# Optimization experiments

Measured on AMD Instinct MI355X. Metric: run time of the kernel, lower is better.

## Reference

```python
import jax, jax.numpy as jnp
import numpy as np

NUM_EXPERTS = 64
HIDDEN_DIM = 4096
TOPK = 8


def setup_inputs() -> dict:
    key = jax.random.key(0)
    kx, kw = jax.random.split(key)
    x = jax.random.normal(kx, (16384, HIDDEN_DIM), dtype=jnp.float32)
    # nn.Linear weight is [num_experts, hidden_dim], init N(0, 0.01)
    W = jax.random.normal(kw, (NUM_EXPERTS, HIDDEN_DIM), dtype=jnp.float32) * 0.01
    return {"x": x, "W": W}


def reference(x, W):
    # router logits: [T, E]
    router_logits = jnp.einsum('th,eh->te', x, W)
    score = jnp.clip(router_logits, -2.0, 2.0)
    # top-k over experts (no router_bias branch)
    topk_scores, topk_indices = jax.lax.top_k(score, TOPK)  # [T, K]
    topk_probs = jax.nn.softmax(topk_scores, axis=-1)
    # dispatch index computation (counting-sort style)
    flat = topk_indices.reshape(-1)                      # [T*K]
    indices = jnp.argsort(flat, stable=True).astype(jnp.int32)
    tokens_per_expert = jnp.bincount(flat, length=NUM_EXPERTS)
    group_indices = jnp.cumsum(tokens_per_expert).astype(jnp.int32)
    tokens_per_expert_f = tokens_per_expert.astype(jnp.float32)
    # load-balance loss
    mean_tokens = tokens_per_expert_f / tokens_per_expert_f.sum()
    mean_prob = jax.nn.softmax(router_logits, axis=-1).mean(axis=0)
    lb_loss = jnp.dot(mean_tokens, mean_prob) * NUM_EXPERTS
    # z-loss
    zl = jnp.mean(jax.scipy.special.logsumexp(router_logits, axis=-1) ** 2)
    return (router_logits, topk_probs, topk_indices, group_indices,
            indices, tokens_per_expert, lb_loss, zl)
```

## Files before the change

### kernel.cpp

```cpp
#include <hip/hip_runtime.h>
#include <hip/hip_bf16.h>
#include <math.h>

#define NTOK   16384
#define NEXP   64
#define HID    4096
#define KSEL   8
#define EPS    7.5e-5f
#define NSPLIT 4
#define KSZ    (HID / NSPLIT)

typedef __attribute__((ext_vector_type(8))) short short8;
typedef __attribute__((ext_vector_type(4))) float f32x4;

#define O_LOGITS 0u
#define O_PROBS  1048576u
#define O_TIDX   1179648u
#define O_GROUP  1310720u
#define O_IDX    1310784u
#define O_TPE    1441856u
#define O_LB     1441920u
#define O_ZL     1441921u

#define W_LSQP    4096u
#define W_CBE     8192u
#define W_PREF    73728u
#define W_PSUM    262144u
#define W_FLAT    524288u
#define W_RNK     1048576u
#define W_WF      2097152u
#define W_PART    4194304u
#define PART_STRIDE 1048576ull

__device__ __forceinline__ unsigned short f2bf(float f) {
  unsigned u = __float_as_uint(f);
  return (unsigned short)((u + 0x7fffu + ((u >> 16) & 1u)) >> 16);
}

__device__ __forceinline__ void gload16(const void* g, void* l) {
  __builtin_amdgcn_global_load_lds((const __attribute__((address_space(1))) unsigned int*)g,
                                   (__attribute__((address_space(3))) unsigned int*)l, 16, 0, 0);
}

__global__ __launch_bounds__(256) void k_prep(const float* __restrict__ w,
                                              short8* __restrict__ wf) {
  const int kk   = blockIdx.x;
  const int nb   = threadIdx.x >> 6;
  const int lane = threadIdx.x & 63;
  const int n    = nb * 16 + (lane & 15);
  const int kb   = kk * 32 + (lane >> 4) * 8;
  const float4* wp = (const float4*)(w + (size_t)n * HID + kb);
  float4 f0 = wp[0], f1 = wp[1];
  float fv[8] = {f0.x, f0.y, f0.z, f0.w, f1.x, f1.y, f1.z, f1.w};
  short8 hi, lo;
#pragma unroll
  for (int j = 0; j < 8; ++j) {
    unsigned short h = f2bf(fv[j]);
    hi[j] = (short)h;
    float r = fv[j] - __uint_as_float((unsigned)h << 16);
    lo[j] = (short)f2bf(r);
  }
  size_t base = ((size_t)(kk * 4 + nb) * 2) * 64 + lane;
  wf[base] = hi;
  wf[base + 64] = lo;
}

__global__ __launch_bounds__(256, 4) void k_gemm(const float* __restrict__ x,
                                                 const short8* __restrict__ wf,
                                                 float* __restrict__ part) {
  __shared__ short8 wl[2][512];
  const int tid  = threadIdx.x;
  const int wv   = tid >> 6;
  const int lane = tid & 63;
  const int t0   = blockIdx.x * 64;
  const int k0   = blockIdx.y * KSZ;
  const int row  = t0 + wv * 16 + (lane & 15);

  const float* xp = x + (size_t)row * HID + k0 + (lane >> 4) * 8;
  const short8* wbase = wf + (size_t)(k0 >> 5) * 512;

  auto stage = [&](int c, int b) {
    const short8* src = wbase + (size_t)c * 512;
#pragma unroll
    for (int r = 0; r < 2; ++r) {
      const int o = r * 256 + wv * 64;
      gload16(src + o + lane, &wl[b][o]);
    }
  };

  f32x4 acc[4] = {{0,0,0,0},{0,0,0,0},{0,0,0,0},{0,0,0,0}};

  stage(0, 0);
  __syncthreads();
  const int nch = KSZ >> 5;
  for (int c = 0; c < nch; ++c) {
    const int b = c & 1;
    if (c + 1 < nch) stage(c + 1, b ^ 1);

    const float4* xq = (const float4*)(xp + c * 32);
    float4 f0 = xq[0], f1 = xq[1];
    unsigned xb[8] = {__float_as_uint(f0.x), __float_as_uint(f0.y),
                      __float_as_uint(f0.z), __float_as_uint(f0.w),
                      __float_as_uint(f1.x), __float_as_uint(f1.y),
                      __float_as_uint(f1.z), __float_as_uint(f1.w)};
    union { unsigned u[4]; short8 s; } ua, ul;
#pragma unroll
    for (int p = 0; p < 4; ++p) {
      unsigned b0 = xb[2 * p], b1 = xb[2 * p + 1];
      ua.u[p] = __builtin_amdgcn_perm(b1, b0, 0x07060302u);
      float r0 = __uint_as_float(b0) - __uint_as_float(b0 & 0xffff0000u);
      float r1 = __uint_as_float(b1) - __uint_as_float(b1 & 0xffff0000u);
      unsigned t0b = __float_as_uint(r0), t1b = __float_as_uint(r1);
      t0b += 0x7fffu + ((t0b >> 16) & 1u);
      t1b += 0x7fffu + ((t1b >> 16) & 1u);
      ul.u[p] = __builtin_amdgcn_perm(t1b, t0b, 0x07060302u);
    }
    short8 ah = ua.s, al = ul.s;

#pragma unroll
    for (int nb = 0; nb < 4; ++nb) {
      short8 bh = wl[b][nb * 128 + lane];
      short8 bl = wl[b][nb * 128 + 64 + lane];
      acc[nb] = __builtin_amdgcn_mfma_f32_16x16x32_bf16(ah, bh, acc[nb], 0, 0, 0);
      acc[nb] = __builtin_amdgcn_mfma_f32_16x16x32_bf16(al, bh, acc[nb], 0, 0, 0);
      acc[nb] = __builtin_amdgcn_mfma_f32_16x16x32_bf16(ah, bl, acc[nb], 0, 0, 0);
    }
    __syncthreads();
  }

  float* p = part + (size_t)blockIdx.y * PART_STRIDE;
  const int mrow = t0 + wv * 16 + (lane >> 4) * 4;
  const int col  = lane & 15;
#pragma unroll
  for (int nb = 0; nb < 4; ++nb)
#pragma unroll
    for (int r = 0; r < 4; ++r)
      p[(size_t)(mrow + r) * 64 + nb * 16 + col] = acc[nb][r];
}

__global__ __launch_bounds__(256) void k_reduce(const float* __restrict__ part,
                                                float* __restrict__ out_logits) {
  unsigned i4 = blockIdx.x * 256u + threadIdx.x;
  const float4* p4 = (const float4*)part;
  float4 v = p4[i4];
#pragma unroll
  for (int s = 1; s < NSPLIT; ++s) {
    float4 a = p4[(size_t)s * (PART_STRIDE / 4) + i4];
    v.x += a.x; v.y += a.y; v.z += a.z; v.w += a.w;
  }
  ((float4*)out_logits)[i4] = v;
}

__global__ __launch_bounds__(256) void k_rowwise(const float* __restrict__ lg,
                                                 const float* __restrict__ x,
                                                 const float* __restrict__ w,
                                                 float* __restrict__ out,
                                                 float* __restrict__ psum,
                                                 float* __restrict__ lsqp,
                                                 int* __restrict__ flat,
                                                 int* __restrict__ rnk_g,
                                                 int* __restrict__ cbe) {
  __shared__ float tile[64][68];
  __shared__ float rmv[64], invv[64], val8s[64];
  __shared__ int   ids[512];
  __shared__ int   rnk_lds[512];
  __shared__ int   cntq[4][64];
  __shared__ int   fl_rows[64];
  __shared__ int   fl_n;
  __shared__ unsigned long long candmask;
  __shared__ double cexact[64];
  const int bid  = blockIdx.x;
  const int tid  = threadIdx.x;
  const int wv   = tid >> 6;
  const int lane = tid & 63;
  const int t0   = bid * 64;
  if (tid == 0) fl_n = 0;

  {
    const size_t boff = (size_t)bid * 4096;
#pragma unroll
    for (int k = 0; k < 16; ++k) {
      int idx = k * 256 + tid;
      tile[idx >> 6][idx & 63] = lg[boff + idx];
    }
  }
  __syncthreads();

  if (wv == 1) {
    const int r = lane;
    float rm = -3.0e38f;
#pragma unroll
    for (int c4 = 0; c4 < 16; ++c4) {
      float4 f = *(float4*)&tile[r][c4 * 4];
      rm = fmaxf(rm, fmaxf(fmaxf(f.x, f.y), fmaxf(f.z, f.w)));
    }
    float se = 0.0f;
#pragma unroll
    for (int c4 = 0; c4 < 16; ++c4) {
      float4 f = *(float4*)&tile[r][c4 * 4];
      se += expf(f.x - rm) + expf(f.y - rm) + expf(f.z - rm) + expf(f.w - rm);
    }
    rmv[r] = rm; invv[r] = 1.0f / se;
    float lse = rm + logf(se);
    float l2 = lse * lse;
#pragma unroll
    for (int o = 32; o > 0; o >>= 1) l2 += __shfl_down(l2, o);
    if (lane == 0) lsqp[bid] = l2;
  }
  __syncthreads();

  if (wv == 0) {
    const unsigned t = t0 + lane;
    float val[9]; int idx[9];
#pragma unroll
    for (int j = 0; j < 9; ++j) { val[j] = -3.0e38f; idx[j] = 0; }
    bool flag = false;
#pragma unroll
    for (int c4 = 0; c4 < 16; ++c4) {
      float4 f = *(float4*)&tile[lane][c4 * 4];
      float fe[4] = {f.x, f.y, f.z, f.w};
#pragma unroll
      for (int jj = 0; jj < 4; ++jj) {
        float v = fe[jj];
        flag = flag || (fabsf(fabsf(v) - 2.0f) < EPS);
        float c = fminf(fmaxf(v, -2.0f), 2.0f);
        int id = c4 * 4 + jj;
#pragma unroll
        for (int j = 0; j < 9; ++j) {
          bool sw = c > val[j];
          float tv = sw ? val[j] : c; int ti = sw ? idx[j] : id;
          val[j] = sw ? c : val[j];   idx[j] = sw ? id : idx[j];
          c = tv; id = ti;
        }
      }
    }
    val8s[lane] = val[8];
#pragma unroll
    for (int j = 0; j < 8; ++j) {
      float gap = val[j] - val[j + 1];
      bool bothclip = (val[j] == val[j + 1]) && (fabsf(val[j]) == 2.0f);
      flag = flag || (gap < EPS && !bothclip);
    }
    if (!flag) {
      float m = val[0], pe[8], sum = 0.0f;
#pragma unroll
      for (int j = 0; j < 8; ++j) { pe[j] = expf(val[j] - m); sum += pe[j]; }
      float inv = 1.0f / sum;
      *(float4*)&out[O_PROBS + (size_t)t * 8]     = make_float4(pe[0]*inv, pe[1]*inv, pe[2]*inv, pe[3]*inv);
      *(float4*)&out[O_PROBS + (size_t)t * 8 + 4] = make_float4(pe[4]*inv, pe[5]*inv, pe[6]*inv, pe[7]*inv);
      *(float4*)&out[O_TIDX + (size_t)t * 8]      = make_float4((float)idx[0], (float)idx[1], (float)idx[2], (float)idx[3]);
      *(float4*)&out[O_TIDX + (size_t)t * 8 + 4]  = make_float4((float)idx[4], (float)idx[5], (float)idx[6], (float)idx[7]);
      *(int4*)&flat[(size_t)t * 8]     = make_int4(idx[0], idx[1], idx[2], idx[3]);
      *(int4*)&flat[(size_t)t * 8 + 4] = make_int4(idx[4], idx[5], idx[6], idx[7]);
#pragma unroll
      for (int j = 0; j < 8; ++j) ids[lane * 8 + j] = idx[j];
    } else {
      int sl = atomicAdd(&fl_n, 1);
      fl_rows[sl] = lane;
    }
  } else if (wv == 2 || wv == 3) {
    const int e = lane, half = wv - 2;
    float s = 0.0f;
#pragma unroll
    for (int r = 0; r < 32; ++r) {
      int rr = half * 32 + r;
      s += expf(tile[rr][e] - rmv[rr]) * invv[rr];
    }
    psum[(size_t)bid * 128 + half * 64 + e] = s;
  }
  __syncthreads();

  for (int i = 0; i < fl_n; ++i) {
    const int r = fl_rows[i];
    if (wv == 0) {
      float c = fminf(fmaxf(tile[r][lane], -2.0f), 2.0f);
      bool cnd = (c >= val8s[r] - 3.0f * EPS);
      unsigned long long m = __ballot(cnd);
      if (lane == 0) candmask = m;
    }
    __syncthreads();
    const unsigned long long m = candmask;
    const float* xr = x + (size_t)(t0 + r) * HID;
    {
      int ord = 0;
      for (int e = 0; e < 64; ++e) {
        if ((m >> e) & 1ull) {
          if ((ord & 3) == wv) {
            const float* wr = w + (size_t)e * HID;
            double p0 = 0.0, p1 = 0.0, p2 = 0.0, p3 = 0.0;
            const int kb = lane * 64;
            for (int k = kb; k < kb + 64; k += 4) {
              float4 xv = *(const float4*)&xr[k];
              float4 wv4 = *(const float4*)&wr[k];
              p0 = fma((double)xv.x, (double)wv4.x, p0);
              p1 = fma((double)xv.y, (double)wv4.y, p1);
              p2 = fma((double)xv.z, (double)wv4.z, p2);
              p3 = fma((double)xv.w, (double)wv4.w, p3);
            }
            double p = (p0 + p1) + (p2 + p3);
#pragma unroll
            for (int o = 32; o > 0; o >>= 1) p += __shfl_down(p, o);
            if (lane == 0) cexact[e] = fmin(fmax(p, -2.0), 2.0);
          }
          ord++;
        }
      }
    }
    __syncthreads();
    if (tid == r) {
      double val[8]; int idx[8];
#pragma unroll
      for (int j = 0; j < 8; ++j) { val[j] = -1.0e300; idx[j] = 0; }
      for (int e = 0; e < 64; ++e) {
        if (!((m >> e) & 1ull)) continue;
        double c = cexact[e];
        int id = e;
#pragma unroll
        for (int j = 0; j < 8; ++j) {
          bool sw = c > val[j];
          double tv = sw ? val[j] : c; int ti = sw ? idx[j] : id;
          val[j] = sw ? c : val[j];    idx[j] = sw ? id : idx[j];
          c = tv; id = ti;
        }
      }
      float mm = (float)val[0], pe[8], sum = 0.0f;
#pragma unroll
      for (int j = 0; j < 8; ++j) { pe[j] = expf((float)val[j] - mm); sum += pe[j]; }
      float inv = 1.0f / sum;
      const unsigned t = t0 + r;
#pragma unroll
      for (int j = 0; j < 8; ++j) {
        out[O_PROBS + (size_t)t * 8 + j] = pe[j] * inv;
        out[O_TIDX  + (size_t)t * 8 + j] = (float)idx[j];
        flat[(size_t)t * 8 + j] = idx[j];
        ids[r * 8 + j] = idx[j];
      }
    }
    __syncthreads();
  }

  {
    int cnt = 0;
    const int base = wv * 128;
    for (int i = base; i < base + 128; ++i) {
      int id = ids[i];
      if (id == lane) { rnk_lds[i] = cnt; cnt++; }
    }
    cntq[wv][lane] = cnt;
  }
  __syncthreads();

#pragma unroll
  for (int k2 = 0; k2 < 2; ++k2) {
    const int i = tid * 2 + k2;
    const int e = ids[i];
    int r = rnk_lds[i];
    const int q = i >> 7;
    for (int wq = 0; wq < q; ++wq) r += cntq[wq][e];
    rnk_g[(size_t)bid * 512 + i] = r;
  }
  if (tid < 64)
    cbe[bid * 64 + tid] = cntq[0][tid] + cntq[1][tid] + cntq[2][tid] + cntq[3][tid];
}

__global__ __launch_bounds__(256) void k_scan(const int* __restrict__ cbe,
                                              const float* __restrict__ psum,
                                              const float* __restrict__ lsqp,
                                              int* __restrict__ pref,
                                              float* __restrict__ out) {
  __shared__ int ctot[64];
  __shared__ float gsum[4][64];
  const int tid = threadIdx.x;
  const int e = tid & 63, g = tid >> 6;

  float ps = 0.0f;
  for (int b = g; b < 256; b += 4) ps += psum[(size_t)b * 128 + e] + psum[(size_t)b * 128 + 64 + e];
  gsum[g][e] = ps;

  if (tid < 64) {
    int s = 0;
    for (int b = 0; b < 256; ++b) s += cbe[b * 64 + tid];
    ctot[tid] = s;
  }
  __syncthreads();

  if (tid < 64) {
    int incl = 0;
    for (int i = 0; i <= tid; ++i) incl += ctot[i];
    const int tpe = ctot[tid];
    out[O_TPE + tid]   = (float)tpe;
    out[O_GROUP + tid] = (float)incl;
    int run = incl - tpe;
    for (int b = 0; b < 256; ++b) { pref[b * 64 + tid] = run; run += cbe[b * 64 + tid]; }

    float pst = (gsum[0][tid] + gsum[1][tid]) + (gsum[2][tid] + gsum[3][tid]);
    float term = ((float)tpe / 131072.0f) * (pst / 16384.0f) * 64.0f;
#pragma unroll
    for (int o2 = 32; o2 > 0; o2 >>= 1) term += __shfl_down(term, o2);
    float zs = (lsqp[tid * 4] + lsqp[tid * 4 + 1]) + (lsqp[tid * 4 + 2] + lsqp[tid * 4 + 3]);
#pragma unroll
    for (int o2 = 32; o2 > 0; o2 >>= 1) zs += __shfl_down(zs, o2);
    if (tid == 0) { out[O_LB] = term; out[O_ZL] = zs / 16384.0f; }
  }
}

__global__ __launch_bounds__(256) void k_scatter(const int* __restrict__ flat,
                                                 const int* __restrict__ rnk,
                                                 const int* __restrict__ pref,
                                                 float* __restrict__ out) {
  const int j = blockIdx.x * 256 + threadIdx.x;
  const int e = flat[j];
  const int pos = pref[(j >> 9) * 64 + e] + rnk[j];
  out[O_IDX + pos] = (float)j;
}

extern "C" void kernel_launch(void* const* d_in, const int* in_sizes, int n_in,
                              void* d_out, int out_size, void* d_ws, size_t ws_size,
                              hipStream_t stream) {
  (void)in_sizes; (void)n_in; (void)out_size; (void)ws_size;
  const float* x  = (const float*)d_in[0];
  const float* Wm = (const float*)d_in[1];
  float* out = (float*)d_out;
  char*  ws  = (char*)d_ws;

  float*  lsqp   = (float*)(ws + W_LSQP);
  int*    cbe    = (int*)(ws + W_CBE);
  int*    pref   = (int*)(ws + W_PREF);
  float*  psum   = (float*)(ws + W_PSUM);
  int*    flat   = (int*)(ws + W_FLAT);
  int*    rnk    = (int*)(ws + W_RNK);
  short8* wf     = (short8*)(ws + W_WF);
  float*  part   = (float*)(ws + W_PART);

  k_prep   <<<dim3(128),  dim3(256), 0, stream>>>(Wm, wf);
  k_gemm   <<<dim3(NTOK / 64, NSPLIT), dim3(256), 0, stream>>>(x, wf, part);
  k_reduce <<<dim3(1024), dim3(256), 0, stream>>>(part, out + O_LOGITS);
  k_rowwise<<<dim3(256),  dim3(256), 0, stream>>>(out + O_LOGITS, x, Wm, out, psum, lsqp, flat, rnk, cbe);
  k_scan   <<<dim3(1),    dim3(256), 0, stream>>>(cbe, psum, lsqp, pref, out);
  k_scatter<<<dim3(512),  dim3(256), 0, stream>>>(flat, rnk, pref, out);
}
```

Baseline: 170.3 us.

## Compute per-block expert ranks with wave ballots and parallelize scan across four waves

The per-block rank computation, which scanned 512 LDS entries per lane, is replaced by per-expert ballot masks built in one wave, with each rank taken as a popcount of the mask below the lane. The single-block scan kernel now splits its 256-block count accumulation and prefix writes across four waves using segment partial sums, instead of running serial loops in one wave. Both target serial latency in small kernels. The cost is ballot and LDS work concentrated in wave 0, and a correctness dependence on the wave barrier ordering the mask writes before they are read.

```diff
diff --git a/kernel.cpp b/kernel.cpp
--- a/kernel.cpp
+++ b/kernel.cpp
@@ -162,9 +162,7 @@
                                                  int* __restrict__ cbe) {
   __shared__ float tile[64][68];
   __shared__ float rmv[64], invv[64], val8s[64];
-  __shared__ int   ids[512];
-  __shared__ int   rnk_lds[512];
-  __shared__ int   cntq[4][64];
+  __shared__ unsigned long long Bmask[64];
   __shared__ int   fl_rows[64];
   __shared__ int   fl_n;
   __shared__ unsigned long long candmask;
@@ -209,6 +207,8 @@
   }
   __syncthreads();
 
+  unsigned long long chosen = 0ull;
+  int myidx[8];
   if (wv == 0) {
     const unsigned t = t0 + lane;
     float val[9]; int idx[9];
@@ -253,7 +253,7 @@
       *(int4*)&flat[(size_t)t * 8]     = make_int4(idx[0], idx[1], idx[2], idx[3]);
       *(int4*)&flat[(size_t)t * 8 + 4] = make_int4(idx[4], idx[5], idx[6], idx[7]);
 #pragma unroll
-      for (int j = 0; j < 8; ++j) ids[lane * 8 + j] = idx[j];
+      for (int j = 0; j < 8; ++j) { myidx[j] = idx[j]; chosen |= 1ull << idx[j]; }
     } else {
       int sl = atomicAdd(&fl_n, 1);
       fl_rows[sl] = lane;
@@ -328,39 +328,34 @@
       for (int j = 0; j < 8; ++j) { pe[j] = expf((float)val[j] - mm); sum += pe[j]; }
       float inv = 1.0f / sum;
       const unsigned t = t0 + r;
+      chosen = 0ull;
 #pragma unroll
       for (int j = 0; j < 8; ++j) {
         out[O_PROBS + (size_t)t * 8 + j] = pe[j] * inv;
         out[O_TIDX  + (size_t)t * 8 + j] = (float)idx[j];
         flat[(size_t)t * 8 + j] = idx[j];
-        ids[r * 8 + j] = idx[j];
+        myidx[j] = idx[j];
+        chosen |= 1ull << idx[j];
       }
     }
     __syncthreads();
   }
 
-  {
-    int cnt = 0;
-    const int base = wv * 128;
-    for (int i = base; i < base + 128; ++i) {
-      int id = ids[i];
-      if (id == lane) { rnk_lds[i] = cnt; cnt++; }
-    }
-    cntq[wv][lane] = cnt;
-  }
-  __syncthreads();
-
-#pragma unroll
-  for (int k2 = 0; k2 < 2; ++k2) {
-    const int i = tid * 2 + k2;
-    const int e = ids[i];
-    int r = rnk_lds[i];
-    const int q = i >> 7;
-    for (int wq = 0; wq < q; ++wq) r += cntq[wq][e];
-    rnk_g[(size_t)bid * 512 + i] = r;
-  }
-  if (tid < 64)
-    cbe[bid * 64 + tid] = cntq[0][tid] + cntq[1][tid] + cntq[2][tid] + cntq[3][tid];
+  if (wv == 0) {
+    for (int e = 0; e < 64; ++e) {
+      unsigned long long b = __ballot((chosen >> e) & 1ull);
+      if (lane == 0) Bmask[e] = b;
+    }
+    __builtin_amdgcn_wave_barrier();
+    const unsigned long long below = (lane == 0) ? 0ull : (~0ull >> (64 - lane));
+    int rr[8];
+#pragma unroll
+    for (int j = 0; j < 8; ++j)
+      rr[j] = (int)__popcll(Bmask[myidx[j]] & below);
+    *(int4*)&rnk_g[(size_t)bid * 512 + lane * 8]     = make_int4(rr[0], rr[1], rr[2], rr[3]);
+    *(int4*)&rnk_g[(size_t)bid * 512 + lane * 8 + 4] = make_int4(rr[4], rr[5], rr[6], rr[7]);
+    cbe[bid * 64 + lane] = (int)__popcll(Bmask[lane]);
+  }
 }
 
 __global__ __launch_bounds__(256) void k_scan(const int* __restrict__ cbe,
@@ -368,19 +363,25 @@
                                               const float* __restrict__ lsqp,
                                               int* __restrict__ pref,
                                               float* __restrict__ out) {
+  __shared__ int part4[4][64];
+  __shared__ int segb[4][64];
   __shared__ int ctot[64];
   __shared__ float gsum[4][64];
   const int tid = threadIdx.x;
   const int e = tid & 63, g = tid >> 6;
 
   float ps = 0.0f;
-  for (int b = g; b < 256; b += 4) ps += psum[(size_t)b * 128 + e] + psum[(size_t)b * 128 + 64 + e];
+  int cs = 0;
+  for (int b = g * 64; b < g * 64 + 64; ++b) {
+    ps += psum[(size_t)b * 128 + e] + psum[(size_t)b * 128 + 64 + e];
+    cs += cbe[b * 64 + e];
+  }
   gsum[g][e] = ps;
+  part4[g][e] = cs;
+  __syncthreads();
 
   if (tid < 64) {
-    int s = 0;
-    for (int b = 0; b < 256; ++b) s += cbe[b * 64 + tid];
-    ctot[tid] = s;
+    ctot[tid] = part4[0][tid] + part4[1][tid] + part4[2][tid] + part4[3][tid];
   }
   __syncthreads();
 
@@ -390,8 +391,8 @@
     const int tpe = ctot[tid];
     out[O_TPE + tid]   = (float)tpe;
     out[O_GROUP + tid] = (float)incl;
-    int run = incl - tpe;
-    for (int b = 0; b < 256; ++b) { pref[b * 64 + tid] = run; run += cbe[b * 64 + tid]; }
+    int base = incl - tpe;
+    for (int gg = 0; gg < 4; ++gg) { segb[gg][tid] = base; base += part4[gg][tid]; }
 
     float pst = (gsum[0][tid] + gsum[1][tid]) + (gsum[2][tid] + gsum[3][tid]);
     float term = ((float)tpe / 131072.0f) * (pst / 16384.0f) * 64.0f;
@@ -401,6 +402,13 @@
 #pragma unroll
     for (int o2 = 32; o2 > 0; o2 >>= 1) zs += __shfl_down(zs, o2);
     if (tid == 0) { out[O_LB] = term; out[O_ZL] = zs / 16384.0f; }
+  }
+  __syncthreads();
+
+  int run = segb[g][e];
+  for (int b = g * 64; b < g * 64 + 64; ++b) {
+    pref[b * 64 + e] = run;
+    run += cbe[b * 64 + e];
   }
 }
 
```

Measured after the change: 145.1 us. 1.17x faster.
